# Optimization experiments

Measured on AMD Instinct MI355X. Metric: run time of the kernel, lower is better.

The kernel has to match this reference:

```python
import jax, jax.numpy as jnp
import numpy as np
from jax import lax

BN_EPS = 1e-5


def ste_sign(t):
    # sign() binarization with straight-through estimator (identity grad),
    # matching BinarizeConv2d which binarizes .data in-place.
    return t + lax.stop_gradient(jnp.sign(t) - t)


def setup_inputs() -> dict:
    key = jax.random.key(0)
    k1, k2, k3, k4 = jax.random.split(key, 4)
    N, C, H, W = 128, 256, 28, 28
    x = jax.random.normal(k1, (N, C, H, W), dtype=jnp.float32)
    w = jax.random.normal(k2, (C, C, 3, 3), dtype=jnp.float32)  # OIHW
    gamma = jnp.ones((C,), dtype=jnp.float32)
    beta = jnp.zeros((C,), dtype=jnp.float32)
    running_mean = jax.random.normal(k3, (C,), dtype=jnp.float32)
    running_var = jax.random.uniform(k4, (C,), dtype=jnp.float32)
    return {"x": x, "w": w, "gamma": gamma, "beta": beta,
            "running_mean": running_mean, "running_var": running_var}


def reference(x, w, gamma, beta, running_mean, running_var):
    residual = x
    # Binarize activations and weights to {-1, 0, +1} via sign (0 measure-zero for randn)
    xb = ste_sign(x)
    wb = ste_sign(w)
    # 3x3 conv, stride 1, padding 1, no bias
    out = lax.conv_general_dilated(
        xb, wb, window_strides=(1, 1), padding=((1, 1), (1, 1)),
        dimension_numbers=("NCHW", "OIHW", "NCHW"))
    # BatchNorm2d (inference form with running stats), per-channel affine
    inv = gamma / jnp.sqrt(running_var + BN_EPS)  # [C]
    out = out * inv[None, :, None, None] + (beta - running_mean * inv)[None, :, None, None]
    # Hardtanh
    out = jnp.clip(out, -1.0, 1.0)
    # residual add (downsample is None)
    return out + residual
```

## Files before the change

### kernel.cpp

```cpp
#include <hip/hip_runtime.h>
#include <stdint.h>

typedef unsigned long long u64;

#define N_ 128
#define C_ 256
#define H_ 28
#define W_ 28
#define BN_EPS_ 1e-5f


__global__ __launch_bounds__(256) void pack_x_kernel(const float* __restrict__ x,
                                                     u64* __restrict__ xbits) {
    int nh = blockIdx.x;
    int h  = nh % H_;
    int n  = nh / H_;
    __shared__ float sx[C_][W_ + 1];

    const float* xplane = x + ((size_t)n * C_ * H_ + h) * W_;
    for (int i = threadIdx.x; i < C_ * 7; i += 256) {
        int c = i / 7, q = i - c * 7;
        float4 v = *(const float4*)(xplane + (size_t)c * (H_ * W_) + q * 4);
        sx[c][q * 4 + 0] = v.x;
        sx[c][q * 4 + 1] = v.y;
        sx[c][q * 4 + 2] = v.z;
        sx[c][q * 4 + 3] = v.w;
    }
    __syncthreads();

    int k    = threadIdx.x >> 6;
    int lane = threadIdx.x & 63;
    int c    = k * 64 + lane;
    u64 my = 0;
    #pragma unroll
    for (int w = 0; w < W_; ++w) {
        u64 mask = __ballot(sx[c][w] < 0.f);
        if (lane == w) my = mask;
    }
    if (lane < W_) xbits[((size_t)nh * W_ + lane) * 4 + k] = my;
}

__global__ __launch_bounds__(256) void pack_w_kernel(const float* __restrict__ w,
                                                     u64* __restrict__ wbits) {
    int gid  = blockIdx.x * blockDim.x + threadIdx.x;
    int wave = gid >> 6;
    int lane = gid & 63;
    if (wave >= C_ * 9 * 4) return;
    int k    = wave & 3;
    int rest = wave >> 2;
    int tap  = rest % 9;
    int co   = rest / 9;
    int ci   = k * 64 + lane;
    float val = w[((size_t)co * C_ + ci) * 9 + tap];
    u64 mask = __ballot(val < 0.f);
    if (lane == 0) wbits[wave] = mask;
}

__global__ __launch_bounds__(512, 4) void conv_kernel(
    const u64* __restrict__ xbits, const u64* __restrict__ wbits,
    const float* __restrict__ x,
    const float* __restrict__ gamma, const float* __restrict__ beta,
    const float* __restrict__ mean, const float* __restrict__ var,
    float* __restrict__ out) {
    int nh = blockIdx.x;
    int h  = nh % H_;
    int n  = nh / H_;
    int co = threadIdx.x >> 1;
    int kh = threadIdx.x & 1;

    __shared__ u64   lx[3][W_][4];
    __shared__ float sout[C_][W_ + 1];

    float inv  = gamma[co] / sqrtf(var[co] + BN_EPS_);
    float bias = beta[co] - mean[co] * inv;

    u64 wr[9][2];
    {
        const u64* wp = wbits + (size_t)co * 36 + kh * 2;
        #pragma unroll
        for (int t = 0; t < 9; ++t) {
            ulonglong2 a = *(const ulonglong2*)(wp + t * 4);
            wr[t][0] = a.x; wr[t][1] = a.y;
        }
    }

    if (threadIdx.x < 3 * W_ * 4) {
        int i    = threadIdx.x;
        int k    = i & 3;
        int rest = i >> 2;
        int ww   = rest % W_;
        int r    = rest / W_;
        int ih   = h - 1 + r;
        u64 v = 0;
        if (ih >= 0 && ih < H_)
            v = xbits[(((size_t)n * H_ + ih) * W_ + ww) * 4 + k];
        lx[r][ww][k] = v;
    }
    __syncthreads();

    const bool row0 = (h > 0);
    const bool row2 = (h < H_ - 1);
    const int  nrows = 1 + (row0 ? 1 : 0) + (row2 ? 1 : 0);
    const int  nv3 = C_ * nrows * 3;
    const int  nv2 = C_ * nrows * 2;

    int pm = 0, pc = 0;

    #pragma unroll 4
    for (int iw = 0; iw < W_; ++iw) {
        int a0 = 0, a1 = 0, a2 = 0;
        ulonglong2 xr;
        #define TAPROW(r, wb)                                                  \
            xr = *(const ulonglong2*)&lx[r][iw][kh * 2];                       \
            a0 += __popcll(xr.x ^ wr[wb+0][0]) + __popcll(xr.y ^ wr[wb+0][1]); \
            a1 += __popcll(xr.x ^ wr[wb+1][0]) + __popcll(xr.y ^ wr[wb+1][1]); \
            a2 += __popcll(xr.x ^ wr[wb+2][0]) + __popcll(xr.y ^ wr[wb+2][1]);
        if (row0) { TAPROW(0, 0) }
        { TAPROW(1, 3) }
        if (row2) { TAPROW(2, 6) }
        #undef TAPROW

        if (iw >= 1) {
            int s = pm + a2;
            s += __shfl_xor(s, 1);
            int nv = (iw == 1) ? nv2 : nv3;
            float val = (float)(nv - 2 * s) * inv + bias;
            val = fminf(1.f, fmaxf(-1.f, val));
            if (kh == 0) sout[co][iw - 1] = val;
        }
        pm = pc + a1;
        pc = a0;
    }
    {
        int s = pm;
        s += __shfl_xor(s, 1);
        float val = (float)(nv2 - 2 * s) * inv + bias;
        val = fminf(1.f, fmaxf(-1.f, val));
        if (kh == 0) sout[co][W_ - 1] = val;
    }
    __syncthreads();

    const float* xplane = x   + ((size_t)n * C_ * H_ + h) * W_;
    float*       oplane = out + ((size_t)n * C_ * H_ + h) * W_;
    for (int i = threadIdx.x; i < C_ * 7; i += 512) {
        int c = i / 7, q = i - c * 7;
        size_t g = (size_t)c * (H_ * W_) + q * 4;
        float4 r = *(const float4*)(xplane + g);
        float4 o;
        o.x = sout[c][q * 4 + 0] + r.x;
        o.y = sout[c][q * 4 + 1] + r.y;
        o.z = sout[c][q * 4 + 2] + r.z;
        o.w = sout[c][q * 4 + 3] + r.w;
        *(float4*)(oplane + g) = o;
    }
}

extern "C" void kernel_launch(void* const* d_in, const int* in_sizes, int n_in,
                              void* d_out, int out_size, void* d_ws, size_t ws_size,
                              hipStream_t stream) {
    const float* x     = (const float*)d_in[0];
    const float* w     = (const float*)d_in[1];
    const float* gamma = (const float*)d_in[2];
    const float* beta  = (const float*)d_in[3];
    const float* mean  = (const float*)d_in[4];
    const float* var   = (const float*)d_in[5];
    float* out = (float*)d_out;

    u64* xbits = (u64*)d_ws;
    u64* wbits = xbits + (size_t)N_ * H_ * W_ * 4;

    pack_x_kernel<<<N_ * H_, 256, 0, stream>>>(x, xbits);
    pack_w_kernel<<<(C_ * 9 * 4 * 64) / 256, 256, 0, stream>>>(w, wbits);
    conv_kernel<<<N_ * H_, 512, 0, stream>>>(xbits, wbits, x, gamma, beta, mean, var, out);
}
```

Before: 320.7 us.

## Replace XOR-popcount conv with int8 MFMA implicit GEMM over padded input

Binarized activations and weights are packed as int8 ±1 values into a zero-padded 30x30 spatial grid, so the 3x3 conv becomes an implicit GEMM: each of the 9 taps is a shifted row offset into the same padded A matrix. The GEMM runs on 32x32x32 i8 MFMA instructions with double-buffered register loads, and the epilogue applies BN, clamp and the residual add through shared memory. This aims to move the dot products from scalar popcount onto the matrix cores. In exchange it computes over padded rows that are then discarded, needs a larger workspace, and writes output with strided, poorly coalesced stores. The old bitpacked path is kept as a fallback when the workspace is too small.

Result: slower. 438.1 us (+36.6%).

```diff
diff --git a/kernel.cpp b/kernel.cpp
--- a/kernel.cpp
+++ b/kernel.cpp
@@ -2,6 +2,8 @@
 #include <stdint.h>
 
 typedef unsigned long long u64;
+typedef int v4i  __attribute__((ext_vector_type(4)));
+typedef int v16i __attribute__((ext_vector_type(16)));
 
 #define N_ 128
 #define C_ 256
@@ -9,6 +11,186 @@
 #define W_ 28
 #define BN_EPS_ 1e-5f
 
+#define GP_ 30
+#define MROWS_ (N_ * GP_ * GP_)
+#define A_BYTES_ ((size_t)(MROWS_ + 64) * C_)
+#define B_BYTES_ ((size_t)9 * C_ * C_)
+
+static __device__ inline v16i vzero16() {
+    v16i v;
+    #pragma unroll
+    for (int i = 0; i < 16; ++i) v[i] = 0;
+    return v;
+}
+
+
+__global__ __launch_bounds__(256) void pack_a_kernel(const float* __restrict__ x,
+                                                     char* __restrict__ A) {
+    int gy = blockIdx.x % GP_;
+    int n  = blockIdx.x / GP_;
+    int* arow = (int*)(A + ((size_t)n * GP_ + gy) * GP_ * C_);
+    if (gy == 0 || gy == GP_ - 1) {
+        for (int i = threadIdx.x; i < GP_ * 64; i += 256) arow[i] = 0;
+        return;
+    }
+    int h = gy - 1;
+    __shared__ float sx[C_][W_ + 1];
+    const float* xplane = x + ((size_t)n * C_ * H_ + h) * W_;
+    for (int i = threadIdx.x; i < C_ * 7; i += 256) {
+        int c = i / 7, q = i - c * 7;
+        float4 v = *(const float4*)(xplane + (size_t)c * (H_ * W_) + q * 4);
+        sx[c][q*4+0] = v.x; sx[c][q*4+1] = v.y;
+        sx[c][q*4+2] = v.z; sx[c][q*4+3] = v.w;
+    }
+    __syncthreads();
+    for (int i = threadIdx.x; i < GP_ * 64; i += 256) {
+        int gx = i >> 6, d = i & 63;
+        unsigned r = 0;
+        if (gx > 0 && gx < GP_ - 1) {
+            int w = gx - 1;
+            unsigned b0 = sx[4*d+0][w] < 0.f ? 0xFFu : 0x01u;
+            unsigned b1 = sx[4*d+1][w] < 0.f ? 0xFFu : 0x01u;
+            unsigned b2 = sx[4*d+2][w] < 0.f ? 0xFFu : 0x01u;
+            unsigned b3 = sx[4*d+3][w] < 0.f ? 0xFFu : 0x01u;
+            r = b0 | (b1 << 8) | (b2 << 16) | (b3 << 24);
+        }
+        arow[i] = (int)r;
+    }
+}
+
+__global__ __launch_bounds__(256) void pack_b_kernel(const float* __restrict__ w,
+                                                     char* __restrict__ B) {
+    int tap = blockIdx.x % 9;
+    int cog = blockIdx.x / 9;
+    int co  = cog * 32 + (threadIdx.x >> 3);
+    int* brow = (int*)(B + ((size_t)tap * C_ + co) * C_);
+    for (int k = 0; k < 8; ++k) {
+        int d = (threadIdx.x & 7) + 8 * k;
+        unsigned r = 0;
+        #pragma unroll
+        for (int j = 0; j < 4; ++j) {
+            int ci = 4 * d + j;
+            float v = w[((size_t)co * C_ + ci) * 9 + tap];
+            r |= (v < 0.f ? 0xFFu : 0x01u) << (8 * j);
+        }
+        brow[d] = (int)r;
+    }
+}
+
+__global__ __launch_bounds__(256, 2) void gemm_kernel(
+    const char* __restrict__ A, const char* __restrict__ B,
+    const float* __restrict__ x,
+    const float* __restrict__ gamma, const float* __restrict__ beta,
+    const float* __restrict__ mean, const float* __restrict__ var,
+    float* __restrict__ out) {
+
+    int t   = threadIdx.x;
+    int wid = t >> 6, lane = t & 63;
+    int wm  = wid & 1, wn = wid >> 1;
+    int l31 = lane & 31, lh = lane >> 5;
+    long bm0 = (long)blockIdx.x * 128;
+
+    __shared__ float sE[32][257];
+
+    float inv_f[4], bias_f[4];
+    #pragma unroll
+    for (int fn = 0; fn < 4; ++fn) {
+        int co = wn * 128 + fn * 32 + l31;
+        float iv = gamma[co] / sqrtf(var[co] + BN_EPS_);
+        inv_f[fn]  = iv;
+        bias_f[fn] = beta[co] - mean[co] * iv;
+    }
+
+    const char* Ab0 = A + (size_t)(bm0 + wm * 64 +  0 + l31) * C_ + lh * 16;
+    const char* Ab1 = A + (size_t)(bm0 + wm * 64 + 32 + l31) * C_ + lh * 16;
+    const char* Bb0 = B + (size_t)(wn * 128 +   0 + l31) * C_ + lh * 16;
+    const char* Bb1 = B + (size_t)(wn * 128 +  32 + l31) * C_ + lh * 16;
+    const char* Bb2 = B + (size_t)(wn * 128 +  64 + l31) * C_ + lh * 16;
+    const char* Bb3 = B + (size_t)(wn * 128 +  96 + l31) * C_ + lh * 16;
+
+    v16i acc00 = vzero16(), acc01 = vzero16(), acc02 = vzero16(), acc03 = vzero16();
+    v16i acc10 = vzero16(), acc11 = vzero16(), acc12 = vzero16(), acc13 = vzero16();
+
+#define LOADK(kk, ra0, ra1, rb0, rb1, rb2, rb3)                                \
+    {                                                                          \
+        int tap_ = (kk) >> 3, s_ = (kk) & 7;                                   \
+        int dh_ = tap_ / 3, dw_ = tap_ - dh_ * 3;                              \
+        size_t ao_ = (size_t)(dh_ * GP_ + dw_) * C_ + (size_t)s_ * 32;         \
+        size_t bo_ = (size_t)tap_ * C_ * C_ + (size_t)s_ * 32;                 \
+        ra0 = *(const v4i*)(Ab0 + ao_);                                        \
+        ra1 = *(const v4i*)(Ab1 + ao_);                                        \
+        rb0 = *(const v4i*)(Bb0 + bo_);                                        \
+        rb1 = *(const v4i*)(Bb1 + bo_);                                        \
+        rb2 = *(const v4i*)(Bb2 + bo_);                                        \
+        rb3 = *(const v4i*)(Bb3 + bo_);                                        \
+    }
+
+#define MFMA8(aa0, aa1, bb0, bb1, bb2, bb3)                                    \
+    acc00 = __builtin_amdgcn_mfma_i32_32x32x32_i8(aa0, bb0, acc00, 0, 0, 0);   \
+    acc01 = __builtin_amdgcn_mfma_i32_32x32x32_i8(aa0, bb1, acc01, 0, 0, 0);   \
+    acc02 = __builtin_amdgcn_mfma_i32_32x32x32_i8(aa0, bb2, acc02, 0, 0, 0);   \
+    acc03 = __builtin_amdgcn_mfma_i32_32x32x32_i8(aa0, bb3, acc03, 0, 0, 0);   \
+    acc10 = __builtin_amdgcn_mfma_i32_32x32x32_i8(aa1, bb0, acc10, 0, 0, 0);   \
+    acc11 = __builtin_amdgcn_mfma_i32_32x32x32_i8(aa1, bb1, acc11, 0, 0, 0);   \
+    acc12 = __builtin_amdgcn_mfma_i32_32x32x32_i8(aa1, bb2, acc12, 0, 0, 0);   \
+    acc13 = __builtin_amdgcn_mfma_i32_32x32x32_i8(aa1, bb3, acc13, 0, 0, 0);
+
+    v4i a0A, a1A, b0A, b1A, b2A, b3A;
+    v4i a0B, a1B, b0B, b1B, b2B, b3B;
+
+    LOADK(0, a0A, a1A, b0A, b1A, b2A, b3A)
+    for (int kk = 0; kk < 72; kk += 2) {
+        LOADK(kk + 1, a0B, a1B, b0B, b1B, b2B, b3B)
+        MFMA8(a0A, a1A, b0A, b1A, b2A, b3A)
+        if (kk + 2 < 72) {
+            LOADK(kk + 2, a0A, a1A, b0A, b1A, b2A, b3A)
+        }
+        MFMA8(a0B, a1B, b0B, b1B, b2B, b3B)
+    }
+#undef LOADK
+#undef MFMA8
+
+#define EPIW(FM, F0, F1, F2, F3)                                               \
+    {                                                                          \
+        _Pragma("unroll")                                                      \
+        for (int fn = 0; fn < 4; ++fn) {                                       \
+            v16i fr = (fn == 0) ? F0 : (fn == 1) ? F1 : (fn == 2) ? F2 : F3;   \
+            _Pragma("unroll")                                                  \
+            for (int r = 0; r < 16; ++r) {                                     \
+                int mloc = (r & 3) + 8 * (r >> 2) + 4 * lh;                    \
+                float val = (float)fr[r] * inv_f[fn] + bias_f[fn];             \
+                val = fminf(1.f, fmaxf(-1.f, val));                            \
+                sE[mloc][wn * 128 + fn * 32 + l31] = val;                      \
+            }                                                                  \
+        }                                                                      \
+    }
+
+    #pragma unroll
+    for (int msub = 0; msub < 4; ++msub) {
+        __syncthreads();
+        if (wm == (msub >> 1)) {
+            if ((msub & 1) == 0) { EPIW(0, acc00, acc01, acc02, acc03) }
+            else                 { EPIW(1, acc10, acc11, acc12, acc13) }
+        }
+        __syncthreads();
+        int mloc = t & 31;
+        int cob  = (t >> 5) * 32;
+        long gm  = bm0 + msub * 32 + mloc;
+        int nimg = (int)(gm / (GP_ * GP_));
+        int rem  = (int)(gm - (long)nimg * (GP_ * GP_));
+        int yy = rem / GP_;
+        int xx = rem - yy * GP_;
+        if (yy < H_ && xx < W_) {
+            size_t g = (((size_t)nimg * C_ + cob) * H_ + yy) * W_ + xx;
+            #pragma unroll
+            for (int k2 = 0; k2 < 32; ++k2) {
+                out[g] = sE[mloc][cob + k2] + x[g];
+                g += (size_t)(H_ * W_);
+            }
+        }
+    }
+#undef EPIW
+}
 
 __global__ __launch_bounds__(256) void pack_x_kernel(const float* __restrict__ x,
                                                      u64* __restrict__ xbits) {
@@ -16,18 +198,13 @@
     int h  = nh % H_;
     int n  = nh / H_;
     __shared__ float sx[C_][W_ + 1];
-
     const float* xplane = x + ((size_t)n * C_ * H_ + h) * W_;
     for (int i = threadIdx.x; i < C_ * 7; i += 256) {
         int c = i / 7, q = i - c * 7;
         float4 v = *(const float4*)(xplane + (size_t)c * (H_ * W_) + q * 4);
-        sx[c][q * 4 + 0] = v.x;
-        sx[c][q * 4 + 1] = v.y;
-        sx[c][q * 4 + 2] = v.z;
-        sx[c][q * 4 + 3] = v.w;
+        sx[c][q*4+0]=v.x; sx[c][q*4+1]=v.y; sx[c][q*4+2]=v.z; sx[c][q*4+3]=v.w;
     }
     __syncthreads();
-
     int k    = threadIdx.x >> 6;
     int lane = threadIdx.x & 63;
     int c    = k * 64 + lane;
@@ -83,7 +260,6 @@
             wr[t][0] = a.x; wr[t][1] = a.y;
         }
     }
-
     if (threadIdx.x < 3 * W_ * 4) {
         int i    = threadIdx.x;
         int k    = i & 3;
@@ -105,7 +281,6 @@
     const int  nv2 = C_ * nrows * 2;
 
     int pm = 0, pc = 0;
-
     #pragma unroll 4
     for (int iw = 0; iw < W_; ++iw) {
         int a0 = 0, a1 = 0, a2 = 0;
@@ -119,7 +294,6 @@
         { TAPROW(1, 3) }
         if (row2) { TAPROW(2, 6) }
         #undef TAPROW
-
         if (iw >= 1) {
             int s = pm + a2;
             s += __shfl_xor(s, 1);
@@ -147,10 +321,10 @@
         size_t g = (size_t)c * (H_ * W_) + q * 4;
         float4 r = *(const float4*)(xplane + g);
         float4 o;
-        o.x = sout[c][q * 4 + 0] + r.x;
-        o.y = sout[c][q * 4 + 1] + r.y;
-        o.z = sout[c][q * 4 + 2] + r.z;
-        o.w = sout[c][q * 4 + 3] + r.w;
+        o.x = sout[c][q*4+0] + r.x;
+        o.y = sout[c][q*4+1] + r.y;
+        o.z = sout[c][q*4+2] + r.z;
+        o.w = sout[c][q*4+3] + r.w;
         *(float4*)(oplane + g) = o;
     }
 }
@@ -166,10 +340,19 @@
     const float* var   = (const float*)d_in[5];
     float* out = (float*)d_out;
 
-    u64* xbits = (u64*)d_ws;
-    u64* wbits = xbits + (size_t)N_ * H_ * W_ * 4;
-
-    pack_x_kernel<<<N_ * H_, 256, 0, stream>>>(x, xbits);
-    pack_w_kernel<<<(C_ * 9 * 4 * 64) / 256, 256, 0, stream>>>(w, wbits);
-    conv_kernel<<<N_ * H_, 512, 0, stream>>>(xbits, wbits, x, gamma, beta, mean, var, out);
-}
+    if (ws_size >= A_BYTES_ + B_BYTES_) {
+        char* Abuf = (char*)d_ws;
+        char* Bbuf = Abuf + A_BYTES_;
+        pack_a_kernel<<<N_ * GP_, 256, 0, stream>>>(x, Abuf);
+        pack_b_kernel<<<9 * 8, 256, 0, stream>>>(w, Bbuf);
+        gemm_kernel<<<MROWS_ / 128, 256, 0, stream>>>(Abuf, Bbuf, x, gamma, beta,
+                                                      mean, var, out);
+    } else {
+        u64* xbits = (u64*)d_ws;
+        u64* wbits = xbits + (size_t)N_ * H_ * W_ * 4;
+        pack_x_kernel<<<N_ * H_, 256, 0, stream>>>(x, xbits);
+        pack_w_kernel<<<(C_ * 9 * 4 * 64) / 256, 256, 0, stream>>>(w, wbits);
+        conv_kernel<<<N_ * H_, 512, 0, stream>>>(xbits, wbits, x, gamma, beta,
+                                                 mean, var, out);
+    }
+}
```
